# Optimization experiments

Hardware: AMD Instinct MI355X
Metric: run time of the kernel (lower is better)

Reference implementation:

```python
import jax, jax.numpy as jnp
from jax import lax
import numpy as np

BN_EPS = 1e-5

def nearest_resize(x, out_h, out_w):
    # torch F.interpolate(mode='nearest'): src = floor(dst * in / out)
    B, C, H, W = x.shape
    hi = (jnp.arange(out_h) * H) // out_h
    wi = (jnp.arange(out_w) * W) // out_w
    return x[:, :, hi][:, :, :, wi]

def conv1x1(x, w, b=None):
    y = jnp.einsum('bchw,oc->bohw', x, w)
    if b is not None:
        y = y + b[None, :, None, None]
    return y

def dwconv(x, w, stride, pad):
    C = x.shape[1]
    return lax.conv_general_dilated(x, w, (stride, stride), [(pad, pad), (pad, pad)],
                                    dimension_numbers=('NCHW', 'OIHW', 'NCHW'),
                                    feature_group_count=C)

def bn(x, g, b, m, v):
    scale = g / jnp.sqrt(v + BN_EPS)
    return (x - m[None, :, None, None]) * scale[None, :, None, None] + b[None, :, None, None]


def setup_inputs() -> dict:
    key = jax.random.key(0)
    ks = jax.random.split(key, 8)
    B, C, H0, W0 = 4, 512, 192, 192
    w_scale = 0.05
    return {
        'x': jax.random.normal(ks[0], (B, C, H0, W0), jnp.float32),
        'q_w': jax.random.normal(ks[1], (C, C), jnp.float32) * w_scale,
        'q_b': jnp.zeros((C,), jnp.float32),
        'kv_w': jax.random.normal(ks[2], (2 * C, C), jnp.float32) * w_scale,
        'kv_b': jnp.zeros((2 * C,), jnp.float32),
        'sr1_w': jax.random.normal(ks[3], (C, 1, 2, 2), jnp.float32) * w_scale,
        'bn1_g': jnp.ones((C,), jnp.float32),
        'bn1_b': jnp.zeros((C,), jnp.float32),
        'bn1_m': jnp.zeros((C,), jnp.float32),
        'bn1_v': jnp.ones((C,), jnp.float32),
        'sr2_w': jax.random.normal(ks[4], (C, C), jnp.float32) * w_scale,
        'bn2_g': jnp.ones((C,), jnp.float32),
        'bn2_b': jnp.zeros((C,), jnp.float32),
        'bn2_m': jnp.zeros((C,), jnp.float32),
        'bn2_v': jnp.ones((C,), jnp.float32),
        'lc_w': jax.random.normal(ks[5], (C, 1, 3, 3), jnp.float32) * w_scale,
        'lc_b': jnp.zeros((C,), jnp.float32),
        'head_num': 8,
    }


def reference(x, q_w, q_b, kv_w, kv_b, sr1_w, bn1_g, bn1_b, bn1_m, bn1_v,
              sr2_w, bn2_g, bn2_b, bn2_m, bn2_v, lc_w, lc_b, head_num):
    origin_h, origin_w = x.shape[2], x.shape[3]
    x = nearest_resize(x, origin_h // 4, origin_w // 4)
    B, C, H, W = x.shape
    hd = C // head_num
    scale = hd ** (-0.5)

    # q projection (1x1 conv with bias)
    q = conv1x1(x, q_w, q_b)  # [B,C,H,W]

    # spatial reduction: depthwise conv(k=sr, s=sr, p=sr//2) + BN + ReLU, then 1x1 + BN
    sr = sr1_w.shape[-1]
    kv = jax.nn.relu(bn(dwconv(x, sr1_w, sr, sr // 2), bn1_g, bn1_b, bn1_m, bn1_v))
    kv = bn(conv1x1(kv, sr2_w), bn2_g, bn2_b, bn2_m, bn2_v)

    # local depthwise 3x3 conv residual
    kv = dwconv(kv, lc_w, 1, 1) + lc_b[None, :, None, None] + kv

    # kv projection (1x1 conv, 2C output)
    kv = conv1x1(kv, kv_w, kv_b)
    k, v = jnp.split(kv, 2, axis=1)  # each [B,C,Hs,Ws]
    M = k.shape[2] * k.shape[3]

    q_ = jnp.swapaxes(q.reshape(B, head_num, hd, H * W), -1, -2)  # [B,h,N,hd]
    k_ = k.reshape(B, head_num, hd, M)                             # [B,h,hd,M]
    v_ = jnp.swapaxes(v.reshape(B, head_num, hd, M), -1, -2)       # [B,h,M,hd]

    attn = jax.nn.softmax(jnp.matmul(q_, k_) * scale, axis=-1)     # [B,h,N,M]
    out = jnp.swapaxes(jnp.matmul(attn, v_), -1, -2).reshape(B, C, H, W)

    # NOTE: original torch code passes size=(origin_w, origin_h)
    out = nearest_resize(out, origin_w, origin_h)
    return out
```

## Files before the change

kernel.cpp:

```cpp
#include <hip/hip_runtime.h>

#define Bsz 4
#define Cc  512
#define C2  1024
#define H0c 192
#define Hh  48
#define Nn  2304
#define HNh 8
#define HD  64
#define Hs  25
#define Ms  625

typedef const float* fp;
typedef _Float16 f16;
typedef __attribute__((ext_vector_type(8))) _Float16 f16x8;
typedef __attribute__((ext_vector_type(4))) _Float16 f16x4;
typedef __attribute__((ext_vector_type(4))) float    f32x4;

__global__ __launch_bounds__(256) void k_cvtw(fp __restrict__ q_w, fp __restrict__ sr2_w,
                                              fp __restrict__ kv_w, f16* __restrict__ wh) {
    int idx = blockIdx.x * 256 + threadIdx.x;
    float v;
    if (idx < 262144)      v = q_w[idx];
    else if (idx < 524288) v = sr2_w[idx - 262144];
    else                   v = kv_w[idx - 524288];
    wh[idx] = (f16)v;
}

__global__ __launch_bounds__(256) void k_ds_t(fp __restrict__ x,
                                              float* __restrict__ xds,
                                              f16* __restrict__ xt) {
    __shared__ float tile[32][33];
    const int b = blockIdx.z;
    const int s0 = blockIdx.x * 32, r0 = blockIdx.y * 32;
    const int t = threadIdx.x;
    const float* xb = x + (size_t)b * Cc * H0c * H0c;
    float* xdsb = xds + (size_t)b * Cc * Nn;
    #pragma unroll
    for (int p = 0; p < 4; p++) {
        int e = t + p * 256; int i = e >> 5, j = e & 31;
        int c = r0 + i, n = s0 + j;
        float v = xb[((size_t)c * H0c + (n / Hh) * 4) * H0c + (n % Hh) * 4];
        tile[i][j] = v;
        xdsb[(size_t)c * Nn + n] = v;
    }
    __syncthreads();
    #pragma unroll
    for (int p = 0; p < 4; p++) {
        int e = t + p * 256; int oi = e >> 5, oj = e & 31;
        xt[((size_t)b * Nn + s0 + oi) * Cc + r0 + oj] = (f16)tile[oj][oi];
    }
}

__global__ __launch_bounds__(256) void k_sr1t(const float* __restrict__ xds,
                                              fp __restrict__ w, fp g, fp bb, fp bm, fp bv,
                                              f16* __restrict__ kv1t) {
    __shared__ float tile[32][33];
    const int b = blockIdx.z;
    const int s0 = blockIdx.x * 32, r0 = blockIdx.y * 32;
    const int t = threadIdx.x;
    #pragma unroll
    for (int p = 0; p < 4; p++) {
        int e = t + p * 256; int i = e >> 5, j = e & 31;
        int c = r0 + i, n = s0 + j;
        float v = 0.f;
        if (n < Ms) {
            int ho = n / Hs, wo = n % Hs;
            const float* src = xds + ((size_t)b * Cc + c) * Nn;
            float acc = 0.f;
            #pragma unroll
            for (int di = 0; di < 2; di++) {
                int ih = ho * 2 - 1 + di;
                if (ih < 0 || ih >= Hh) continue;
                #pragma unroll
                for (int dj = 0; dj < 2; dj++) {
                    int iw = wo * 2 - 1 + dj;
                    if (iw < 0 || iw >= Hh) continue;
                    acc += w[c * 4 + di * 2 + dj] * src[ih * Hh + iw];
                }
            }
            float sc = g[c] * rsqrtf(bv[c] + 1e-5f);
            v = fmaxf((acc - bm[c]) * sc + bb[c], 0.f);
        }
        tile[i][j] = v;
    }
    __syncthreads();
    #pragma unroll
    for (int p = 0; p < 4; p++) {
        int e = t + p * 256; int oi = e >> 5, oj = e & 31;
        if (s0 + oi < Ms)
            kv1t[((size_t)b * Ms + s0 + oi) * Cc + r0 + oj] = (f16)tile[oj][oi];
    }
}

__global__ __launch_bounds__(256) void k_lct(const float* __restrict__ kv2,
                                             fp __restrict__ w, fp __restrict__ lb,
                                             f16* __restrict__ kv3t) {
    __shared__ float tile[32][33];
    const int b = blockIdx.z;
    const int s0 = blockIdx.x * 32, r0 = blockIdx.y * 32;
    const int t = threadIdx.x;
    #pragma unroll
    for (int p = 0; p < 4; p++) {
        int e = t + p * 256; int i = e >> 5, j = e & 31;
        int c = r0 + i, n = s0 + j;
        float v = 0.f;
        if (n < Ms) {
            int ho = n / Hs, wo = n % Hs;
            const float* src = kv2 + ((size_t)b * Cc + c) * Ms;
            float acc = 0.f;
            #pragma unroll
            for (int di = 0; di < 3; di++) {
                int ih = ho - 1 + di;
                if (ih < 0 || ih >= Hs) continue;
                #pragma unroll
                for (int dj = 0; dj < 3; dj++) {
                    int iw = wo - 1 + dj;
                    if (iw < 0 || iw >= Hs) continue;
                    acc += w[c * 9 + di * 3 + dj] * src[ih * Hs + iw];
                }
            }
            v = acc + lb[c] + src[n];
        }
        tile[i][j] = v;
    }
    __syncthreads();
    #pragma unroll
    for (int p = 0; p < 4; p++) {
        int e = t + p * 256; int oi = e >> 5, oj = e & 31;
        if (s0 + oi < Ms)
            kv3t[((size_t)b * Ms + s0 + oi) * Cc + r0 + oj] = (f16)tile[oj][oi];
    }
}

__global__ __launch_bounds__(256) void k_gemm_mfma(
    const f16* __restrict__ W, const f16* __restrict__ Xt,
    float* __restrict__ Yf, f16* __restrict__ Yt, f16* __restrict__ Vt,
    const int Md, const int Nd, const int NtRows, const int mode, const float oscale,
    fp __restrict__ bias,
    fp __restrict__ bn_g, fp __restrict__ bn_b, fp __restrict__ bn_m, fp __restrict__ bn_v)
{
    __shared__ f16 sA[128 * 80];
    __shared__ f16 sB[128 * 80];
    const int b  = blockIdx.z;
    const int m0 = blockIdx.y * 128, n0 = blockIdx.x * 128;
    const int t = threadIdx.x;
    const int lane = t & 63, w = t >> 6;
    const int lm = lane & 15, q = lane >> 4;
    const int wm = w >> 1, wn = w & 1;
    const f16* Xb = Xt + (size_t)b * Nd * 512;

    f32x4 acc[4][4];
    #pragma unroll
    for (int i = 0; i < 4; i++)
        #pragma unroll
        for (int j = 0; j < 4; j++)
            #pragma unroll
            for (int r = 0; r < 4; r++) acc[i][j][r] = 0.f;

    for (int k0 = 0; k0 < 512; k0 += 64) {
        {
            int r = t >> 1, hh = (t & 1) * 32;
            const f16* wr = W + (size_t)(m0 + r) * 512 + k0 + hh;
            f16* dst = &sA[r * 80 + hh];
            #pragma unroll
            for (int i = 0; i < 4; i++)
                *(f16x8*)&dst[i * 8] = *(const f16x8*)&wr[i * 8];
        }
        {
            int r = t >> 1, hh = (t & 1) * 32;
            bool ok = (n0 + r) < Nd;
            const f16* xr = Xb + (size_t)(n0 + r) * 512 + k0 + hh;
            f16* dst = &sB[r * 80 + hh];
            #pragma unroll
            for (int i = 0; i < 4; i++) {
                f16x8 v;
                if (ok) {
                    v = *(const f16x8*)&xr[i * 8];
                } else {
                    for (int z = 0; z < 8; z++) v[z] = (f16)0.f;
                }
                *(f16x8*)&dst[i * 8] = v;
            }
        }
        __syncthreads();
        #pragma unroll
        for (int ks = 0; ks < 2; ks++) {
            f16x8 af[4], bf[4];
            #pragma unroll
            for (int i = 0; i < 4; i++)
                af[i] = *(const f16x8*)&sA[(wm * 64 + i * 16 + lm) * 80 + ks * 32 + q * 8];
            #pragma unroll
            for (int j = 0; j < 4; j++)
                bf[j] = *(const f16x8*)&sB[(wn * 64 + j * 16 + lm) * 80 + ks * 32 + q * 8];
            #pragma unroll
            for (int i = 0; i < 4; i++)
                #pragma unroll
                for (int j = 0; j < 4; j++)
                    acc[i][j] = __builtin_amdgcn_mfma_f32_16x16x32_f16(af[i], bf[j], acc[i][j], 0, 0, 0);
        }
        __syncthreads();
    }

    #pragma unroll
    for (int i = 0; i < 4; i++) {
        int ob = m0 + wm * 64 + i * 16 + q * 4;
        float badd[4], bsc[4], bsh[4];
        #pragma unroll
        for (int r = 0; r < 4; r++) {
            int o = ob + r;
            badd[r] = bias ? bias[o] : 0.f;
            if (bn_g) { bsc[r] = bn_g[o] * rsqrtf(bn_v[o] + 1e-5f); bsh[r] = bn_b[o] - bn_m[o] * bsc[r]; }
            else      { bsc[r] = 1.f; bsh[r] = 0.f; }
        }
        #pragma unroll
        for (int j = 0; j < 4; j++) {
            int n = n0 + wn * 64 + j * 16 + lm;
            f32x4 a = acc[i][j];
            if (mode == 0) {
                if (n < Nd) {
                    #pragma unroll
                    for (int r = 0; r < 4; r++)
                        Yf[((size_t)b * Md + ob + r) * Nd + n] = (a[r] + badd[r]) * bsc[r] + bsh[r];
                }
            } else if (mode == 1 || (mode == 2 && ob < 512)) {
                f16x4 h;
                #pragma unroll
                for (int r = 0; r < 4; r++) h[r] = (f16)((a[r] + badd[r]) * oscale);
                int hh = ob >> 6, d0 = ob & 63;
                *(f16x4*)&Yt[((size_t)(b * 8 + hh) * NtRows + n) * 64 + d0] = h;
            } else {
                #pragma unroll
                for (int r = 0; r < 4; r++) {
                    float val = (n < Nd) ? (a[r] + badd[r]) : 0.f;
                    Vt[((size_t)b * Cc + (ob + r - 512)) * 640 + n] = (f16)val;
                }
            }
        }
    }
}

__global__ __launch_bounds__(256) void k_attn_mfma(
    const f16* __restrict__ Qt, const f16* __restrict__ Kt,
    const f16* __restrict__ Vt, float* __restrict__ Obuf)
{
    __shared__ f16 sK[64 * 80];
    __shared__ f16 sV[64 * 80];
    __shared__ f16 sP[4][16 * 80];

    int bh = blockIdx.y;
    int n0 = blockIdx.x * 64;
    int t = threadIdx.x, w = t >> 6, lane = t & 63;
    int lm = lane & 15, q = lane >> 4;
    f16* sPw = &sP[w][0];

    f16x8 qf[2];
    {
        const f16* qrow = Qt + ((size_t)bh * Nn + n0 + w * 16 + lm) * 64;
        qf[0] = *(const f16x8*)&qrow[q * 8];
        qf[1] = *(const f16x8*)&qrow[32 + q * 8];
    }

    f32x4 od[4];
    #pragma unroll
    for (int dt = 0; dt < 4; dt++)
        #pragma unroll
        for (int r = 0; r < 4; r++) od[dt][r] = 0.f;
    float mold[4], lold[4];
    #pragma unroll
    for (int r = 0; r < 4; r++) { mold[r] = -1e30f; lold[r] = 0.f; }

    int kr = t >> 2, kc = t & 3;
    const f16* kbase = Kt + (size_t)bh * 640 * 64;
    const f16* vbase = Vt + (size_t)bh * 64 * 640;

    for (int mc = 0; mc < 640; mc += 64) {
        {
            const f16* ksrc = kbase + (size_t)(mc + kr) * 64;
            *(f16x8*)&sK[kr * 80 + kc * 8]      = *(const f16x8*)&ksrc[kc * 8];
            *(f16x8*)&sK[kr * 80 + 32 + kc * 8] = *(const f16x8*)&ksrc[32 + kc * 8];
            const f16* vsrc = vbase + (size_t)kr * 640 + mc;
            *(f16x8*)&sV[kr * 80 + kc * 8]      = *(const f16x8*)&vsrc[kc * 8];
            *(f16x8*)&sV[kr * 80 + 32 + kc * 8] = *(const f16x8*)&vsrc[32 + kc * 8];
        }
        __syncthreads();

        f32x4 sc4[4];
        #pragma unroll
        for (int j = 0; j < 4; j++)
            #pragma unroll
            for (int r = 0; r < 4; r++) sc4[j][r] = 0.f;
        #pragma unroll
        for (int ks = 0; ks < 2; ks++) {
            #pragma unroll
            for (int j = 0; j < 4; j++) {
                f16x8 kf = *(const f16x8*)&sK[(j * 16 + lm) * 80 + ks * 32 + q * 8];
                sc4[j] = __builtin_amdgcn_mfma_f32_16x16x32_f16(qf[ks], kf, sc4[j], 0, 0, 0);
            }
        }

        const bool lastc = (mc >= 576);
        #pragma unroll
        for (int reg = 0; reg < 4; reg++) {
            float mx;
            if (lastc) {
                mx = -1e30f;
                #pragma unroll
                for (int j = 0; j < 4; j++) {
                    float s = sc4[j][reg];
                    if (576 + j * 16 + lm >= Ms) s = -1e30f;
                    sc4[j][reg] = s;
                    mx = fmaxf(mx, s);
                }
            } else {
                mx = fmaxf(fmaxf(sc4[0][reg], sc4[1][reg]),
                           fmaxf(sc4[2][reg], sc4[3][reg]));
            }
            #pragma unroll
            for (int off = 1; off < 16; off <<= 1) mx = fmaxf(mx, __shfl_xor(mx, off));
            float mnew = fmaxf(mold[reg], mx);
            float alpha = __expf(mold[reg] - mnew);
            float rs = 0.f;
            #pragma unroll
            for (int j = 0; j < 4; j++) {
                float p = __expf(sc4[j][reg] - mnew);
                sc4[j][reg] = p;
                rs += p;
            }
            #pragma unroll
            for (int off = 1; off < 16; off <<= 1) rs += __shfl_xor(rs, off);
            lold[reg] = lold[reg] * alpha + rs;
            mold[reg] = mnew;
            #pragma unroll
            for (int dt = 0; dt < 4; dt++) od[dt][reg] *= alpha;
            #pragma unroll
            for (int j = 0; j < 4; j++)
                sPw[(q * 4 + reg) * 80 + j * 16 + lm] = (f16)sc4[j][reg];
        }

        #pragma unroll
        for (int ks = 0; ks < 2; ks++) {
            f16x8 pa = *(const f16x8*)&sPw[lm * 80 + ks * 32 + q * 8];
            #pragma unroll
            for (int dt = 0; dt < 4; dt++) {
                f16x8 vf = *(const f16x8*)&sV[(dt * 16 + lm) * 80 + ks * 32 + q * 8];
                od[dt] = __builtin_amdgcn_mfma_f32_16x16x32_f16(pa, vf, od[dt], 0, 0, 0);
            }
        }
        __syncthreads();
    }

    float inv[4];
    #pragma unroll
    for (int r = 0; r < 4; r++) inv[r] = 1.f / lold[r];
    #pragma unroll
    for (int dt = 0; dt < 4; dt++) {
        f32x4 o;
        #pragma unroll
        for (int r = 0; r < 4; r++) o[r] = od[dt][r] * inv[r];
        size_t c = (size_t)bh * 64 + dt * 16 + lm;
        *(f32x4*)&Obuf[c * Nn + n0 + w * 16 + q * 4] = o;
    }
}

__global__ __launch_bounds__(256) void k_upsample(const float* __restrict__ O,
                                                  float* __restrict__ out) {
    size_t idx = (size_t)blockIdx.x * 256 + threadIdx.x;
    if (idx >= (size_t)Bsz * Cc * H0c * 48) return;
    int jg = (int)(idx % 48);
    int i  = (int)((idx / 48) % H0c);
    int bc = (int)(idx / ((size_t)48 * H0c));
    float s = O[(size_t)bc * Nn + (i >> 2) * Hh + jg];
    float4 pack = make_float4(s, s, s, s);
    *(float4*)(out + ((size_t)bc * H0c + i) * H0c + jg * 4) = pack;
}

extern "C" void kernel_launch(void* const* d_in, const int* in_sizes, int n_in,
                              void* d_out, int out_size, void* d_ws, size_t ws_size,
                              hipStream_t stream) {
    (void)in_sizes; (void)n_in; (void)out_size; (void)ws_size;
    fp x     = (fp)d_in[0];
    fp q_w   = (fp)d_in[1];
    fp q_b   = (fp)d_in[2];
    fp kv_w  = (fp)d_in[3];
    fp kv_b  = (fp)d_in[4];
    fp sr1_w = (fp)d_in[5];
    fp bn1_g = (fp)d_in[6];
    fp bn1_b = (fp)d_in[7];
    fp bn1_m = (fp)d_in[8];
    fp bn1_v = (fp)d_in[9];
    fp sr2_w = (fp)d_in[10];
    fp bn2_g = (fp)d_in[11];
    fp bn2_b = (fp)d_in[12];
    fp bn2_m = (fp)d_in[13];
    fp bn2_v = (fp)d_in[14];
    fp lc_w  = (fp)d_in[15];
    fp lc_b  = (fp)d_in[16];
    float* out = (float*)d_out;

    float* ws   = (float*)d_ws;
    float* xds  = ws;
    float* Obuf = ws;
    float* kv2  = ws + 4718592;
    f16*   Kt   = (f16*)(ws + 5998592);
    f16*   vt   = (f16*)(ws + 6653952);
    f16*   xt   = (f16*)(ws + 7309312);
    f16*   kv1t = xt;
    f16*   kv3t = xt;
    f16*   Qt   = (f16*)(ws + 9668608);
    f16*   wh   = (f16*)(ws + 12027904);

    k_cvtw<<<4096, 256, 0, stream>>>(q_w, sr2_w, kv_w, wh);
    k_ds_t<<<dim3(72, 16, Bsz), 256, 0, stream>>>(x, xds, xt);
    k_gemm_mfma<<<dim3(18, 4, Bsz), 256, 0, stream>>>(wh, xt, nullptr, Qt, nullptr,
        Cc, Nn, Nn, 1, 0.125f, q_b, nullptr, nullptr, nullptr, nullptr);
    k_sr1t<<<dim3(20, 16, Bsz), 256, 0, stream>>>(xds, sr1_w, bn1_g, bn1_b, bn1_m, bn1_v, kv1t);
    k_gemm_mfma<<<dim3(5, 4, Bsz), 256, 0, stream>>>(wh + 262144, kv1t, kv2, nullptr, nullptr,
        Cc, Ms, 0, 0, 1.f, nullptr, bn2_g, bn2_b, bn2_m, bn2_v);
    k_lct<<<dim3(20, 16, Bsz), 256, 0, stream>>>(kv2, lc_w, lc_b, kv3t);
    k_gemm_mfma<<<dim3(5, 8, Bsz), 256, 0, stream>>>(wh + 524288, kv3t, nullptr, Kt, vt,
        C2, Ms, 640, 2, 1.f, kv_b, nullptr, nullptr, nullptr, nullptr);
    k_attn_mfma<<<dim3(Nn / 64, Bsz * HNh), 256, 0, stream>>>(Qt, Kt, vt, Obuf);
    k_upsample<<<(unsigned)((size_t)Bsz * Cc * H0c * 48 / 256), 256, 0, stream>>>(Obuf, out);
}
```

Before: 617.2 us.

## Process two query subtiles per wave in attention, vectorize weight cast, grid-stride upsample

The attention kernel now covers 128 queries per block: each wave handles two 16-row query subtiles and reuses the same K/V tiles in shared memory, halving the K/V reloads and barriers per query. The weight conversion kernel moves to float4 loads with four fp16 stores per thread on a quarter-size grid. The upsample kernel becomes a grid-stride loop over a fixed 2048-block grid. The attention change doubles the accumulator and softmax-state registers per wave and halves the block count to 576, which may lower occupancy.

```diff
diff --git a/kernel.cpp b/kernel.cpp
--- a/kernel.cpp
+++ b/kernel.cpp
@@ -19,12 +19,13 @@
 
 __global__ __launch_bounds__(256) void k_cvtw(fp __restrict__ q_w, fp __restrict__ sr2_w,
                                               fp __restrict__ kv_w, f16* __restrict__ wh) {
-    int idx = blockIdx.x * 256 + threadIdx.x;
-    float v;
-    if (idx < 262144)      v = q_w[idx];
-    else if (idx < 524288) v = sr2_w[idx - 262144];
-    else                   v = kv_w[idx - 524288];
-    wh[idx] = (f16)v;
+    int i4 = (blockIdx.x * 256 + threadIdx.x) * 4;
+    float4 v;
+    if (i4 < 262144)      v = *(const float4*)&q_w[i4];
+    else if (i4 < 524288) v = *(const float4*)&sr2_w[i4 - 262144];
+    else                  v = *(const float4*)&kv_w[i4 - 524288];
+    f16x4 h; h[0] = (f16)v.x; h[1] = (f16)v.y; h[2] = (f16)v.z; h[3] = (f16)v.w;
+    *(f16x4*)&wh[i4] = h;
 }
 
 __global__ __launch_bounds__(256) void k_ds_t(fp __restrict__ x,
@@ -249,26 +250,29 @@
     __shared__ f16 sP[4][16 * 80];
 
     int bh = blockIdx.y;
-    int n0 = blockIdx.x * 64;
+    int n0 = blockIdx.x * 128;
     int t = threadIdx.x, w = t >> 6, lane = t & 63;
     int lm = lane & 15, q = lane >> 4;
     f16* sPw = &sP[w][0];
 
-    f16x8 qf[2];
-    {
-        const f16* qrow = Qt + ((size_t)bh * Nn + n0 + w * 16 + lm) * 64;
-        qf[0] = *(const f16x8*)&qrow[q * 8];
-        qf[1] = *(const f16x8*)&qrow[32 + q * 8];
-    }
-
-    f32x4 od[4];
-    #pragma unroll
-    for (int dt = 0; dt < 4; dt++)
-        #pragma unroll
-        for (int r = 0; r < 4; r++) od[dt][r] = 0.f;
-    float mold[4], lold[4];
-    #pragma unroll
-    for (int r = 0; r < 4; r++) { mold[r] = -1e30f; lold[r] = 0.f; }
+    f16x8 qf[2][2];
+    #pragma unroll
+    for (int s = 0; s < 2; s++) {
+        const f16* qrow = Qt + ((size_t)bh * Nn + n0 + w * 32 + s * 16 + lm) * 64;
+        qf[s][0] = *(const f16x8*)&qrow[q * 8];
+        qf[s][1] = *(const f16x8*)&qrow[32 + q * 8];
+    }
+
+    f32x4 od[2][4];
+    float mold[2][4], lold[2][4];
+    #pragma unroll
+    for (int s = 0; s < 2; s++)
+        #pragma unroll
+        for (int r = 0; r < 4; r++) {
+            #pragma unroll
+            for (int dt = 0; dt < 4; dt++) od[s][dt][r] = 0.f;
+            mold[s][r] = -1e30f; lold[s][r] = 0.f;
+        }
 
     int kr = t >> 2, kc = t & 3;
     const f16* kbase = Kt + (size_t)bh * 640 * 64;
@@ -285,94 +289,102 @@
         }
         __syncthreads();
 
-        f32x4 sc4[4];
-        #pragma unroll
-        for (int j = 0; j < 4; j++)
-            #pragma unroll
-            for (int r = 0; r < 4; r++) sc4[j][r] = 0.f;
-        #pragma unroll
-        for (int ks = 0; ks < 2; ks++) {
-            #pragma unroll
-            for (int j = 0; j < 4; j++) {
-                f16x8 kf = *(const f16x8*)&sK[(j * 16 + lm) * 80 + ks * 32 + q * 8];
-                sc4[j] = __builtin_amdgcn_mfma_f32_16x16x32_f16(qf[ks], kf, sc4[j], 0, 0, 0);
-            }
-        }
-
         const bool lastc = (mc >= 576);
         #pragma unroll
-        for (int reg = 0; reg < 4; reg++) {
-            float mx;
-            if (lastc) {
-                mx = -1e30f;
+        for (int s = 0; s < 2; s++) {
+            f32x4 sc4[4];
+            #pragma unroll
+            for (int j = 0; j < 4; j++)
+                #pragma unroll
+                for (int r = 0; r < 4; r++) sc4[j][r] = 0.f;
+            #pragma unroll
+            for (int ks = 0; ks < 2; ks++) {
                 #pragma unroll
                 for (int j = 0; j < 4; j++) {
-                    float s = sc4[j][reg];
-                    if (576 + j * 16 + lm >= Ms) s = -1e30f;
-                    sc4[j][reg] = s;
-                    mx = fmaxf(mx, s);
-                }
-            } else {
-                mx = fmaxf(fmaxf(sc4[0][reg], sc4[1][reg]),
-                           fmaxf(sc4[2][reg], sc4[3][reg]));
-            }
-            #pragma unroll
-            for (int off = 1; off < 16; off <<= 1) mx = fmaxf(mx, __shfl_xor(mx, off));
-            float mnew = fmaxf(mold[reg], mx);
-            float alpha = __expf(mold[reg] - mnew);
-            float rs = 0.f;
-            #pragma unroll
-            for (int j = 0; j < 4; j++) {
-                float p = __expf(sc4[j][reg] - mnew);
-                sc4[j][reg] = p;
-                rs += p;
-            }
-            #pragma unroll
-            for (int off = 1; off < 16; off <<= 1) rs += __shfl_xor(rs, off);
-            lold[reg] = lold[reg] * alpha + rs;
-            mold[reg] = mnew;
-            #pragma unroll
-            for (int dt = 0; dt < 4; dt++) od[dt][reg] *= alpha;
-            #pragma unroll
-            for (int j = 0; j < 4; j++)
-                sPw[(q * 4 + reg) * 80 + j * 16 + lm] = (f16)sc4[j][reg];
-        }
-
-        #pragma unroll
-        for (int ks = 0; ks < 2; ks++) {
-            f16x8 pa = *(const f16x8*)&sPw[lm * 80 + ks * 32 + q * 8];
-            #pragma unroll
-            for (int dt = 0; dt < 4; dt++) {
-                f16x8 vf = *(const f16x8*)&sV[(dt * 16 + lm) * 80 + ks * 32 + q * 8];
-                od[dt] = __builtin_amdgcn_mfma_f32_16x16x32_f16(pa, vf, od[dt], 0, 0, 0);
+                    f16x8 kf = *(const f16x8*)&sK[(j * 16 + lm) * 80 + ks * 32 + q * 8];
+                    sc4[j] = __builtin_amdgcn_mfma_f32_16x16x32_f16(qf[s][ks], kf, sc4[j], 0, 0, 0);
+                }
+            }
+
+            #pragma unroll
+            for (int reg = 0; reg < 4; reg++) {
+                float mx;
+                if (lastc) {
+                    mx = -1e30f;
+                    #pragma unroll
+                    for (int j = 0; j < 4; j++) {
+                        float sv = sc4[j][reg];
+                        if (576 + j * 16 + lm >= Ms) sv = -1e30f;
+                        sc4[j][reg] = sv;
+                        mx = fmaxf(mx, sv);
+                    }
+                } else {
+                    mx = fmaxf(fmaxf(sc4[0][reg], sc4[1][reg]),
+                               fmaxf(sc4[2][reg], sc4[3][reg]));
+                }
+                #pragma unroll
+                for (int off = 1; off < 16; off <<= 1) mx = fmaxf(mx, __shfl_xor(mx, off));
+                float mnew = fmaxf(mold[s][reg], mx);
+                float alpha = __expf(mold[s][reg] - mnew);
+                float rs = 0.f;
+                #pragma unroll
+                for (int j = 0; j < 4; j++) {
+                    float p = __expf(sc4[j][reg] - mnew);
+                    sc4[j][reg] = p;
+                    rs += p;
+                }
+                #pragma unroll
+                for (int off = 1; off < 16; off <<= 1) rs += __shfl_xor(rs, off);
+                lold[s][reg] = lold[s][reg] * alpha + rs;
+                mold[s][reg] = mnew;
+                #pragma unroll
+                for (int dt = 0; dt < 4; dt++) od[s][dt][reg] *= alpha;
+                #pragma unroll
+                for (int j = 0; j < 4; j++)
+                    sPw[(q * 4 + reg) * 80 + j * 16 + lm] = (f16)sc4[j][reg];
+            }
+
+            #pragma unroll
+            for (int ks = 0; ks < 2; ks++) {
+                f16x8 pa = *(const f16x8*)&sPw[lm * 80 + ks * 32 + q * 8];
+                #pragma unroll
+                for (int dt = 0; dt < 4; dt++) {
+                    f16x8 vf = *(const f16x8*)&sV[(dt * 16 + lm) * 80 + ks * 32 + q * 8];
+                    od[s][dt] = __builtin_amdgcn_mfma_f32_16x16x32_f16(pa, vf, od[s][dt], 0, 0, 0);
+                }
             }
         }
         __syncthreads();
     }
 
-    float inv[4];
-    #pragma unroll
-    for (int r = 0; r < 4; r++) inv[r] = 1.f / lold[r];
-    #pragma unroll
-    for (int dt = 0; dt < 4; dt++) {
-        f32x4 o;
-        #pragma unroll
-        for (int r = 0; r < 4; r++) o[r] = od[dt][r] * inv[r];
-        size_t c = (size_t)bh * 64 + dt * 16 + lm;
-        *(f32x4*)&Obuf[c * Nn + n0 + w * 16 + q * 4] = o;
+    #pragma unroll
+    for (int s = 0; s < 2; s++) {
+        float inv[4];
+        #pragma unroll
+        for (int r = 0; r < 4; r++) inv[r] = 1.f / lold[s][r];
+        #pragma unroll
+        for (int dt = 0; dt < 4; dt++) {
+            f32x4 o;
+            #pragma unroll
+            for (int r = 0; r < 4; r++) o[r] = od[s][dt][r] * inv[r];
+            size_t c = (size_t)bh * 64 + dt * 16 + lm;
+            *(f32x4*)&Obuf[c * Nn + n0 + w * 32 + s * 16 + q * 4] = o;
+        }
     }
 }
 
 __global__ __launch_bounds__(256) void k_upsample(const float* __restrict__ O,
                                                   float* __restrict__ out) {
-    size_t idx = (size_t)blockIdx.x * 256 + threadIdx.x;
-    if (idx >= (size_t)Bsz * Cc * H0c * 48) return;
-    int jg = (int)(idx % 48);
-    int i  = (int)((idx / 48) % H0c);
-    int bc = (int)(idx / ((size_t)48 * H0c));
-    float s = O[(size_t)bc * Nn + (i >> 2) * Hh + jg];
-    float4 pack = make_float4(s, s, s, s);
-    *(float4*)(out + ((size_t)bc * H0c + i) * H0c + jg * 4) = pack;
+    const size_t total = (size_t)Bsz * Cc * H0c * 48;
+    for (size_t idx = (size_t)blockIdx.x * 256 + threadIdx.x; idx < total;
+         idx += (size_t)gridDim.x * 256) {
+        int jg = (int)(idx % 48);
+        int i  = (int)((idx / 48) % H0c);
+        int bc = (int)(idx / ((size_t)48 * H0c));
+        float s = O[(size_t)bc * Nn + (i >> 2) * Hh + jg];
+        float4 pack = make_float4(s, s, s, s);
+        *(float4*)(out + ((size_t)bc * H0c + i) * H0c + jg * 4) = pack;
+    }
 }
 
 extern "C" void kernel_launch(void* const* d_in, const int* in_sizes, int n_in,
@@ -410,7 +422,7 @@
     f16*   Qt   = (f16*)(ws + 9668608);
     f16*   wh   = (f16*)(ws + 12027904);
 
-    k_cvtw<<<4096, 256, 0, stream>>>(q_w, sr2_w, kv_w, wh);
+    k_cvtw<<<1024, 256, 0, stream>>>(q_w, sr2_w, kv_w, wh);
     k_ds_t<<<dim3(72, 16, Bsz), 256, 0, stream>>>(x, xds, xt);
     k_gemm_mfma<<<dim3(18, 4, Bsz), 256, 0, stream>>>(wh, xt, nullptr, Qt, nullptr,
         Cc, Nn, Nn, 1, 0.125f, q_b, nullptr, nullptr, nullptr, nullptr);
@@ -420,6 +432,6 @@
     k_lct<<<dim3(20, 16, Bsz), 256, 0, stream>>>(kv2, lc_w, lc_b, kv3t);
     k_gemm_mfma<<<dim3(5, 8, Bsz), 256, 0, stream>>>(wh + 524288, kv3t, nullptr, Kt, vt,
         C2, Ms, 640, 2, 1.f, kv_b, nullptr, nullptr, nullptr, nullptr);
-    k_attn_mfma<<<dim3(Nn / 64, Bsz * HNh), 256, 0, stream>>>(Qt, Kt, vt, Obuf);
-    k_upsample<<<(unsigned)((size_t)Bsz * Cc * H0c * 48 / 256), 256, 0, stream>>>(Obuf, out);
-}
+    k_attn_mfma<<<dim3(Nn / 128, Bsz * HNh), 256, 0, stream>>>(Qt, Kt, vt, Obuf);
+    k_upsample<<<2048, 256, 0, stream>>>(Obuf, out);
+}
```

New measurement: 623.3 us. Within noise of the previous version (+1.0%).
